# Kernel optimization log

Measured on AMD Instinct MI355X. Metric: run time of the kernel, lower is better.

The kernel has to match this reference:

```python
import jax, jax.numpy as jnp
import numpy as np

N, D_IN, D_OUT, RANK, MAX_LORAS = 4096, 2048, 2048, 16, 32


def setup_inputs() -> dict:
    key = jax.random.key(0)
    ks = jax.random.split(key, 6)
    x = jax.random.normal(ks[0], (N, D_IN), dtype=jnp.float32)
    adapter_ids = jax.random.randint(ks[1], (N,), 0, MAX_LORAS, dtype=jnp.int32)
    W_base = jax.random.normal(ks[2], (D_OUT, D_IN), dtype=jnp.float32) * (D_IN ** -0.5)
    b_base = jax.random.normal(ks[3], (D_OUT,), dtype=jnp.float32) * 0.01
    lora_A = jax.random.normal(ks[4], (MAX_LORAS, RANK, D_IN), dtype=jnp.float32) * (D_IN ** -0.5)
    lora_B = jax.random.normal(ks[5], (MAX_LORAS, D_OUT, RANK), dtype=jnp.float32) * (RANK ** -0.5)
    lora_scaling = jnp.ones((MAX_LORAS,), dtype=jnp.float32)
    return {"x": x, "adapter_ids": adapter_ids, "W_base": W_base, "b_base": b_base,
            "lora_A": lora_A, "lora_B": lora_B, "lora_scaling": lora_scaling}


def reference(x, adapter_ids, W_base, b_base, lora_A, lora_B, lora_scaling):
    previous_dtype = x.dtype
    # base_layer(x): dense Linear
    result = x @ W_base.T + b_base                      # [N, D_OUT]
    # lora_A(x, adapter_ids): per-token gathered low-rank down-projection (bgmv)
    A_w = lora_A[adapter_ids]                           # [N, RANK, D_IN]
    A_result = jnp.einsum('ni,nri->nr', x, A_w)         # [N, RANK]
    # lora_B(A_result, adapter_ids): per-token gathered up-projection
    B_w = lora_B[adapter_ids]                           # [N, D_OUT, RANK]
    B_result = jnp.einsum('nr,nor->no', A_result, B_w)  # [N, D_OUT]
    # scaled residual add, per-adapter scaling
    scaling = lora_scaling[adapter_ids][:, None]        # [N, 1]
    result = result + B_result * scaling
    # cast back to input dtype (skip_dtype_convert=False)
    return result.astype(previous_dtype)
```

## Files before the change

### kernel.cpp

```cpp
#include <hip/hip_runtime.h>
#include <hip/hip_bf16.h>
#include <stdint.h>

#define NTOK 4096
#define DIN  2048
#define DOUT 2048
#define RANK 16
#define NLORA 32
#define LCAP 512

typedef __attribute__((ext_vector_type(4))) float f32x4;
typedef __attribute__((ext_vector_type(8))) _Float16 f16x8;

typedef const __attribute__((address_space(1))) void* gas_ptr;
typedef __attribute__((address_space(3))) void* las_ptr;

__global__ __launch_bounds__(256)
void prep_kernel(const float* __restrict__ x, const int* __restrict__ ids,
                 const float* __restrict__ W, const float* __restrict__ lA,
                 const float* __restrict__ lB,
                 _Float16* __restrict__ xh, _Float16* __restrict__ wh,
                 _Float16* __restrict__ lAh, _Float16* __restrict__ lBh,
                 int* __restrict__ list, int* __restrict__ counts) {
    const int bid = blockIdx.x;
    if (bid < 7168) {
        const float* src; _Float16* dst; int lb;
        if      (bid < 2048) { src = W;  dst = wh;  lb = bid; }
        else if (bid < 6144) { src = x;  dst = xh;  lb = bid - 2048; }
        else if (bid < 6656) { src = lA; dst = lAh; lb = bid - 6144; }
        else                 { src = lB; dst = lBh; lb = bid - 6656; }
        const size_t i = ((size_t)lb * 256 + threadIdx.x) * 8;
        f32x4 a = *(const f32x4*)(src + i);
        f32x4 b = *(const f32x4*)(src + i + 4);
        f16x8 h;
        h[0] = (_Float16)a.x; h[1] = (_Float16)a.y; h[2] = (_Float16)a.z; h[3] = (_Float16)a.w;
        h[4] = (_Float16)b.x; h[5] = (_Float16)b.y; h[6] = (_Float16)b.z; h[7] = (_Float16)b.w;
        *(f16x8*)(dst + i) = h;
        return;
    }
    const int a = bid - 7168;
    const int wv = threadIdx.x >> 6;
    const int lane = threadIdx.x & 63;
    __shared__ int wcnt[4];
    int c = 0;
    for (int t0 = wv * 1024; t0 < wv * 1024 + 1024; t0 += 64)
        c += __popcll(__ballot(ids[t0 + lane] == a));
    if (lane == 0) wcnt[wv] = c;
    __syncthreads();
    int off = 0;
    for (int w = 0; w < wv; w++) off += wcnt[w];
    if (threadIdx.x == 0) counts[a] = wcnt[0] + wcnt[1] + wcnt[2] + wcnt[3];
    for (int t0 = wv * 1024; t0 < wv * 1024 + 1024; t0 += 64) {
        const int t = t0 + lane;
        const bool m = (ids[t] == a);
        unsigned long long bal = __ballot(m);
        if (m) {
            int pos = off + __popcll(bal & ((1ULL << lane) - 1));
            if (pos < LCAP) list[a * LCAP + pos] = t;
        }
        off += __popcll(bal);
    }
}

__global__ __launch_bounds__(512)
void lora_a_kernel(const _Float16* __restrict__ xh, const _Float16* __restrict__ lAh,
                   const float* __restrict__ scal, const int* __restrict__ list,
                   const int* __restrict__ counts, _Float16* __restrict__ aresh) {
    const int a = blockIdx.x, tile = blockIdx.y;
    const int cnt = counts[a];
    if (tile * 16 >= cnt) return;
    const int wave = threadIdx.x >> 6;
    const int lane = threadIdx.x & 63;
    const int fr = lane & 15, fq = lane >> 4;

    const int idxA = tile * 16 + fr;
    const int tA = (idxA < cnt) ? list[a * LCAP + idxA] : list[a * LCAP];

    const _Float16* xr = xh + (size_t)tA * DIN + wave * 256 + fq * 8;
    const _Float16* ar = lAh + (size_t)a * RANK * DIN + fr * DIN + wave * 256 + fq * 8;

    f32x4 acc = (f32x4){0.f, 0.f, 0.f, 0.f};
#pragma unroll
    for (int st = 0; st < 8; st++) {
        f16x8 af = *(const f16x8*)(xr + st * 32);
        f16x8 bf = *(const f16x8*)(ar + st * 32);
        acc = __builtin_amdgcn_mfma_f32_16x16x32_f16(af, bf, acc, 0, 0, 0);
    }

    __shared__ float red[8][256];
#pragma unroll
    for (int j = 0; j < 4; j++) red[wave][lane * 4 + j] = acc[j];
    __syncthreads();
    if (wave == 0) {
        const float s = scal[a];
#pragma unroll
        for (int j = 0; j < 4; j++) {
            float v = 0.f;
#pragma unroll
            for (int w = 0; w < 8; w++) v += red[w][lane * 4 + j];
            const int m = fq * 4 + j;
            const int idx = tile * 16 + m;
            if (idx < cnt) {
                const int t = list[a * LCAP + idx];
                aresh[(size_t)t * RANK + fr] = (_Float16)(v * s);
            }
        }
    }
}

__global__ __launch_bounds__(512)
void lora_b_kernel(const _Float16* __restrict__ aresh, const _Float16* __restrict__ lBh,
                   const float* __restrict__ bias, const int* __restrict__ list,
                   const int* __restrict__ counts, _Float16* __restrict__ Bresh) {
    const int a = blockIdx.x, tile = blockIdx.y;
    const int cnt = counts[a];
    if (tile * 16 >= cnt) return;
    const int wave = threadIdx.x >> 6;
    const int lane = threadIdx.x & 63;
    const int fr = lane & 15, fq = lane >> 4;

    const int idxA = tile * 16 + fr;
    const int tA = (idxA < cnt) ? list[a * LCAP + idxA] : list[a * LCAP];
    f16x8 af = {};
    if (fq < 2) af = *(const f16x8*)(aresh + (size_t)tA * RANK + fq * 8);

    int tj[4];
#pragma unroll
    for (int j = 0; j < 4; j++) {
        const int idx = tile * 16 + fq * 4 + j;
        tj[j] = (idx < cnt) ? list[a * LCAP + idx] : -1;
    }

    const _Float16* Bb = lBh + (size_t)a * DOUT * RANK;
    for (int oi = 0; oi < 16; oi++) {
        const int ot = oi * 8 + wave;
        const int o = ot * 16 + fr;
        f16x8 bf = {};
        if (fq < 2) bf = *(const f16x8*)(Bb + (size_t)o * RANK + fq * 8);
        f32x4 c = (f32x4){0.f, 0.f, 0.f, 0.f};
        c = __builtin_amdgcn_mfma_f32_16x16x32_f16(af, bf, c, 0, 0, 0);
        const float bv = bias[o];
#pragma unroll
        for (int j = 0; j < 4; j++)
            if (tj[j] >= 0) Bresh[(size_t)tj[j] * DOUT + o] = (_Float16)(c[j] + bv);
    }
}

#define BM 256
#define BN 128
#define BK 32

__global__ __launch_bounds__(512, 2)
void gemm_kernel(const _Float16* __restrict__ Ah, const _Float16* __restrict__ Wh,
                 const _Float16* __restrict__ Bresh, float* __restrict__ out) {
    extern __shared__ _Float16 sm[];
    _Float16* As = sm;
    _Float16* Bs = sm + 16384;

    const int tid = threadIdx.x;
    const int wave = tid >> 6;
    const int lane = tid & 63;
    const int wr = wave >> 1, wc = wave & 1;

    const int p = blockIdx.y * gridDim.x + blockIdx.x;
    const int L = (p & 7) * 32 + (p >> 3);
    const int bm = (L >> 4) * BM;
    const int bn = (L & 15) * BN;

    const int rsub = lane >> 2;
    const int cch = (lane & 3) ^ (rsub & 3);
    const _Float16* srcA[2];
    const _Float16* srcB;
    {
        const int rowA0 = (wave * 2 + 0) * 16 + rsub;
        const int rowA1 = (wave * 2 + 1) * 16 + rsub;
        srcA[0] = Ah + (size_t)(bm + rowA0) * DIN + cch * 8;
        srcA[1] = Ah + (size_t)(bm + rowA1) * DIN + cch * 8;
        const int rowB = wave * 16 + rsub;
        srcB = Wh + (size_t)(bn + rowB) * DIN + cch * 8;
    }

    const int fr = lane & 15;
    const int fq = lane >> 4;
    const int aoff = (wr * 64 + fr) * 32 + ((fq ^ (fr & 3)) * 8);
    const int boff = (wc * 64 + fr) * 32 + ((fq ^ (fr & 3)) * 8);

    f32x4 acc[4][4];
#pragma unroll
    for (int i = 0; i < 4; i++)
#pragma unroll
        for (int j = 0; j < 4; j++) acc[i][j] = (f32x4){0.f, 0.f, 0.f, 0.f};

#define STAGE(buf, koff)                                                                  \
    do {                                                                                  \
        __builtin_amdgcn_global_load_lds((gas_ptr)(srcA[0] + (koff)),                     \
            (las_ptr)(As + (buf) * 8192 + (wave * 2 + 0) * 512), 16, 0, 0);               \
        __builtin_amdgcn_global_load_lds((gas_ptr)(srcA[1] + (koff)),                     \
            (las_ptr)(As + (buf) * 8192 + (wave * 2 + 1) * 512), 16, 0, 0);               \
        __builtin_amdgcn_global_load_lds((gas_ptr)(srcB + (koff)),                        \
            (las_ptr)(Bs + (buf) * 4096 + wave * 512), 16, 0, 0);                         \
    } while (0)

    STAGE(0, 0);
    __syncthreads();

    for (int kt = 0; kt < DIN / BK; ++kt) {
        const int cur = kt & 1;
        if (kt < DIN / BK - 1) STAGE(cur ^ 1, (kt + 1) * BK);

        const _Float16* Ab = As + cur * 8192;
        const _Float16* Bb = Bs + cur * 4096;
        f16x8 ah[4], bh[4];
#pragma unroll
        for (int mi = 0; mi < 4; mi++) ah[mi] = *(const f16x8*)(Ab + aoff + mi * 512);
#pragma unroll
        for (int ni = 0; ni < 4; ni++) bh[ni] = *(const f16x8*)(Bb + boff + ni * 512);
#pragma unroll
        for (int mi = 0; mi < 4; mi++)
#pragma unroll
            for (int ni = 0; ni < 4; ni++)
                acc[mi][ni] = __builtin_amdgcn_mfma_f32_16x16x32_f16(ah[mi], bh[ni], acc[mi][ni], 0, 0, 0);
        __syncthreads();
    }

#pragma unroll
    for (int mi = 0; mi < 4; mi++) {
#pragma unroll
        for (int j = 0; j < 4; j++) {
            const int n = bm + wr * 64 + mi * 16 + fq * 4 + j;
#pragma unroll
            for (int ni = 0; ni < 4; ni++) {
                const int o = bn + wc * 64 + ni * 16 + fr;
                out[(size_t)n * DOUT + o] = acc[mi][ni][j] + (float)Bresh[(size_t)n * DOUT + o];
            }
        }
    }
}

extern "C" void kernel_launch(void* const* d_in, const int* in_sizes, int n_in,
                              void* d_out, int out_size, void* d_ws, size_t ws_size,
                              hipStream_t stream) {
    const float* x    = (const float*)d_in[0];
    const int*   ids  = (const int*)d_in[1];
    const float* W    = (const float*)d_in[2];
    const float* bias = (const float*)d_in[3];
    const float* lA   = (const float*)d_in[4];
    const float* lB   = (const float*)d_in[5];
    const float* scal = (const float*)d_in[6];
    float* out = (float*)d_out;

    _Float16* xh    = (_Float16*)d_ws;
    _Float16* wh    = xh + (size_t)NTOK * DIN;
    _Float16* lAh   = wh + (size_t)DOUT * DIN;
    _Float16* lBh   = lAh + (size_t)NLORA * RANK * DIN;
    _Float16* aresh = lBh + (size_t)NLORA * DOUT * RANK;
    _Float16* Bresh = aresh + (size_t)NTOK * RANK;
    int* list   = (int*)(Bresh + (size_t)NTOK * DOUT);
    int* counts = list + (size_t)NLORA * LCAP;

    prep_kernel<<<dim3(7168 + NLORA), 256, 0, stream>>>(
        x, ids, W, lA, lB, xh, wh, lAh, lBh, list, counts);
    lora_a_kernel<<<dim3(NLORA, 32), 512, 0, stream>>>(
        xh, lAh, scal, list, counts, aresh);
    lora_b_kernel<<<dim3(NLORA, 32), 512, 0, stream>>>(
        aresh, lBh, bias, list, counts, Bresh);
    gemm_kernel<<<dim3(16, 16), 512, 48 * 1024, stream>>>(
        xh, wh, Bresh, out);
}
```

Before: 177.7 us.

## Fuse LoRA A/B kernels and retile base GEMM to 128x128x64 with 256 threads

Merges the LoRA down- and up-projection kernels into one, keeping the rank-16 intermediate in shared memory instead of writing it to global memory. The change removes one launch and the global round trip for the intermediate. The base GEMM is retiled from 256x128 tiles with BK=32 and 512 threads to 128x128 tiles with BK=64 and 256 threads, using 512 blocks. It also switches to an XOR swizzle over 8 slots, explicit vmcnt waits with raw s_barrier, and setprio around the MFMA blocks. The partial vmcnt wait and barrier ordering add risk of races if the counts are wrong.

```diff
diff --git a/kernel.cpp b/kernel.cpp
--- a/kernel.cpp
+++ b/kernel.cpp
@@ -63,9 +63,10 @@
 }
 
 __global__ __launch_bounds__(512)
-void lora_a_kernel(const _Float16* __restrict__ xh, const _Float16* __restrict__ lAh,
-                   const float* __restrict__ scal, const int* __restrict__ list,
-                   const int* __restrict__ counts, _Float16* __restrict__ aresh) {
+void lora_fused_kernel(const _Float16* __restrict__ xh, const _Float16* __restrict__ lAh,
+                       const _Float16* __restrict__ lBh, const float* __restrict__ bias,
+                       const float* __restrict__ scal, const int* __restrict__ list,
+                       const int* __restrict__ counts, _Float16* __restrict__ Bresh) {
     const int a = blockIdx.x, tile = blockIdx.y;
     const int cnt = counts[a];
     if (tile * 16 >= cnt) return;
@@ -73,12 +74,14 @@
     const int lane = threadIdx.x & 63;
     const int fr = lane & 15, fq = lane >> 4;
 
+    __shared__ float red[8][256];
+    __shared__ _Float16 ares_h[16 * 16];
+
     const int idxA = tile * 16 + fr;
     const int tA = (idxA < cnt) ? list[a * LCAP + idxA] : list[a * LCAP];
 
     const _Float16* xr = xh + (size_t)tA * DIN + wave * 256 + fq * 8;
     const _Float16* ar = lAh + (size_t)a * RANK * DIN + fr * DIN + wave * 256 + fq * 8;
-
     f32x4 acc = (f32x4){0.f, 0.f, 0.f, 0.f};
 #pragma unroll
     for (int st = 0; st < 8; st++) {
@@ -86,8 +89,6 @@
         f16x8 bf = *(const f16x8*)(ar + st * 32);
         acc = __builtin_amdgcn_mfma_f32_16x16x32_f16(af, bf, acc, 0, 0, 0);
     }
-
-    __shared__ float red[8][256];
 #pragma unroll
     for (int j = 0; j < 4; j++) red[wave][lane * 4 + j] = acc[j];
     __syncthreads();
@@ -98,43 +99,23 @@
             float v = 0.f;
 #pragma unroll
             for (int w = 0; w < 8; w++) v += red[w][lane * 4 + j];
-            const int m = fq * 4 + j;
-            const int idx = tile * 16 + m;
-            if (idx < cnt) {
-                const int t = list[a * LCAP + idx];
-                aresh[(size_t)t * RANK + fr] = (_Float16)(v * s);
-            }
-        }
-    }
-}
-
-__global__ __launch_bounds__(512)
-void lora_b_kernel(const _Float16* __restrict__ aresh, const _Float16* __restrict__ lBh,
-                   const float* __restrict__ bias, const int* __restrict__ list,
-                   const int* __restrict__ counts, _Float16* __restrict__ Bresh) {
-    const int a = blockIdx.x, tile = blockIdx.y;
-    const int cnt = counts[a];
-    if (tile * 16 >= cnt) return;
-    const int wave = threadIdx.x >> 6;
-    const int lane = threadIdx.x & 63;
-    const int fr = lane & 15, fq = lane >> 4;
-
-    const int idxA = tile * 16 + fr;
-    const int tA = (idxA < cnt) ? list[a * LCAP + idxA] : list[a * LCAP];
+            ares_h[(fq * 4 + j) * RANK + fr] = (_Float16)(v * s);
+        }
+    }
+    __syncthreads();
+
     f16x8 af = {};
-    if (fq < 2) af = *(const f16x8*)(aresh + (size_t)tA * RANK + fq * 8);
-
+    if (fq < 2) af = *(const f16x8*)(ares_h + fr * RANK + fq * 8);
     int tj[4];
 #pragma unroll
     for (int j = 0; j < 4; j++) {
         const int idx = tile * 16 + fq * 4 + j;
         tj[j] = (idx < cnt) ? list[a * LCAP + idx] : -1;
     }
-
     const _Float16* Bb = lBh + (size_t)a * DOUT * RANK;
+#pragma unroll 4
     for (int oi = 0; oi < 16; oi++) {
-        const int ot = oi * 8 + wave;
-        const int o = ot * 16 + fr;
+        const int o = (wave * 16 + oi) * 16 + fr;
         f16x8 bf = {};
         if (fq < 2) bf = *(const f16x8*)(Bb + (size_t)o * RANK + fq * 8);
         f32x4 c = (f32x4){0.f, 0.f, 0.f, 0.f};
@@ -146,11 +127,10 @@
     }
 }
 
-#define BM 256
-#define BN 128
-#define BK 32
-
-__global__ __launch_bounds__(512, 2)
+#define GBK 64
+#define NT (DIN / GBK)
+
+__global__ __launch_bounds__(256, 2)
 void gemm_kernel(const _Float16* __restrict__ Ah, const _Float16* __restrict__ Wh,
                  const _Float16* __restrict__ Bresh, float* __restrict__ out) {
     extern __shared__ _Float16 sm[];
@@ -162,28 +142,24 @@
     const int lane = tid & 63;
     const int wr = wave >> 1, wc = wave & 1;
 
-    const int p = blockIdx.y * gridDim.x + blockIdx.x;
-    const int L = (p & 7) * 32 + (p >> 3);
-    const int bm = (L >> 4) * BM;
-    const int bn = (L & 15) * BN;
-
-    const int rsub = lane >> 2;
-    const int cch = (lane & 3) ^ (rsub & 3);
-    const _Float16* srcA[2];
-    const _Float16* srcB;
-    {
-        const int rowA0 = (wave * 2 + 0) * 16 + rsub;
-        const int rowA1 = (wave * 2 + 1) * 16 + rsub;
-        srcA[0] = Ah + (size_t)(bm + rowA0) * DIN + cch * 8;
-        srcA[1] = Ah + (size_t)(bm + rowA1) * DIN + cch * 8;
-        const int rowB = wave * 16 + rsub;
-        srcB = Wh + (size_t)(bn + rowB) * DIN + cch * 8;
+    const int p = blockIdx.x;
+    const int L = (p & 7) * 64 + (p >> 3);
+    const int bm = (L >> 4) * 128;
+    const int bn = (L & 15) * 128;
+
+    const int rsub = lane >> 3;
+    const int cch = (lane & 7) ^ rsub;
+    const _Float16* srcA[4];
+    const _Float16* srcB[4];
+#pragma unroll
+    for (int i = 0; i < 4; i++) {
+        const int row = (wave * 4 + i) * 8 + rsub;
+        srcA[i] = Ah + (size_t)(bm + row) * DIN + cch * 8;
+        srcB[i] = Wh + (size_t)(bn + row) * DIN + cch * 8;
     }
 
     const int fr = lane & 15;
     const int fq = lane >> 4;
-    const int aoff = (wr * 64 + fr) * 32 + ((fq ^ (fr & 3)) * 8);
-    const int boff = (wc * 64 + fr) * 32 + ((fq ^ (fr & 3)) * 8);
 
     f32x4 acc[4][4];
 #pragma unroll
@@ -193,34 +169,54 @@
 
 #define STAGE(buf, koff)                                                                  \
     do {                                                                                  \
-        __builtin_amdgcn_global_load_lds((gas_ptr)(srcA[0] + (koff)),                     \
-            (las_ptr)(As + (buf) * 8192 + (wave * 2 + 0) * 512), 16, 0, 0);               \
-        __builtin_amdgcn_global_load_lds((gas_ptr)(srcA[1] + (koff)),                     \
-            (las_ptr)(As + (buf) * 8192 + (wave * 2 + 1) * 512), 16, 0, 0);               \
-        __builtin_amdgcn_global_load_lds((gas_ptr)(srcB + (koff)),                        \
-            (las_ptr)(Bs + (buf) * 4096 + wave * 512), 16, 0, 0);                         \
+        _Pragma("unroll")                                                                 \
+        for (int i = 0; i < 4; i++) {                                                     \
+            __builtin_amdgcn_global_load_lds((gas_ptr)(srcA[i] + (koff)),                 \
+                (las_ptr)(As + (buf) * 8192 + (wave * 4 + i) * 512), 16, 0, 0);           \
+            __builtin_amdgcn_global_load_lds((gas_ptr)(srcB[i] + (koff)),                 \
+                (las_ptr)(Bs + (buf) * 8192 + (wave * 4 + i) * 512), 16, 0, 0);           \
+        }                                                                                 \
     } while (0)
 
     STAGE(0, 0);
-    __syncthreads();
-
-    for (int kt = 0; kt < DIN / BK; ++kt) {
+
+    for (int kt = 0; kt < NT; ++kt) {
         const int cur = kt & 1;
-        if (kt < DIN / BK - 1) STAGE(cur ^ 1, (kt + 1) * BK);
+        if (kt < NT - 1) {
+            STAGE(cur ^ 1, (kt + 1) * GBK);
+            asm volatile("s_waitcnt vmcnt(8)" ::: "memory");
+        } else {
+            asm volatile("s_waitcnt vmcnt(0)" ::: "memory");
+        }
+        __builtin_amdgcn_s_barrier();
+        __builtin_amdgcn_sched_barrier(0);
 
         const _Float16* Ab = As + cur * 8192;
-        const _Float16* Bb = Bs + cur * 4096;
-        f16x8 ah[4], bh[4];
-#pragma unroll
-        for (int mi = 0; mi < 4; mi++) ah[mi] = *(const f16x8*)(Ab + aoff + mi * 512);
-#pragma unroll
-        for (int ni = 0; ni < 4; ni++) bh[ni] = *(const f16x8*)(Bb + boff + ni * 512);
-#pragma unroll
-        for (int mi = 0; mi < 4; mi++)
-#pragma unroll
-            for (int ni = 0; ni < 4; ni++)
-                acc[mi][ni] = __builtin_amdgcn_mfma_f32_16x16x32_f16(ah[mi], bh[ni], acc[mi][ni], 0, 0, 0);
-        __syncthreads();
+        const _Float16* Bb = Bs + cur * 8192;
+#pragma unroll
+        for (int kk = 0; kk < 2; kk++) {
+            f16x8 av[4], bv[4];
+#pragma unroll
+            for (int mi = 0; mi < 4; mi++) {
+                const int row = wr * 64 + mi * 16 + fr;
+                const int slot = (kk * 4 + fq) ^ (row & 7);
+                av[mi] = *(const f16x8*)(Ab + row * 64 + slot * 8);
+            }
+#pragma unroll
+            for (int ni = 0; ni < 4; ni++) {
+                const int row = wc * 64 + ni * 16 + fr;
+                const int slot = (kk * 4 + fq) ^ (row & 7);
+                bv[ni] = *(const f16x8*)(Bb + row * 64 + slot * 8);
+            }
+            __builtin_amdgcn_s_setprio(1);
+#pragma unroll
+            for (int mi = 0; mi < 4; mi++)
+#pragma unroll
+                for (int ni = 0; ni < 4; ni++)
+                    acc[mi][ni] = __builtin_amdgcn_mfma_f32_16x16x32_f16(av[mi], bv[ni], acc[mi][ni], 0, 0, 0);
+            __builtin_amdgcn_s_setprio(0);
+        }
+        __builtin_amdgcn_s_barrier();
     }
 
 #pragma unroll
@@ -253,17 +249,14 @@
     _Float16* wh    = xh + (size_t)NTOK * DIN;
     _Float16* lAh   = wh + (size_t)DOUT * DIN;
     _Float16* lBh   = lAh + (size_t)NLORA * RANK * DIN;
-    _Float16* aresh = lBh + (size_t)NLORA * DOUT * RANK;
-    _Float16* Bresh = aresh + (size_t)NTOK * RANK;
+    _Float16* Bresh = lBh + (size_t)NLORA * DOUT * RANK;
     int* list   = (int*)(Bresh + (size_t)NTOK * DOUT);
     int* counts = list + (size_t)NLORA * LCAP;
 
     prep_kernel<<<dim3(7168 + NLORA), 256, 0, stream>>>(
         x, ids, W, lA, lB, xh, wh, lAh, lBh, list, counts);
-    lora_a_kernel<<<dim3(NLORA, 32), 512, 0, stream>>>(
-        xh, lAh, scal, list, counts, aresh);
-    lora_b_kernel<<<dim3(NLORA, 32), 512, 0, stream>>>(
-        aresh, lBh, bias, list, counts, Bresh);
-    gemm_kernel<<<dim3(16, 16), 512, 48 * 1024, stream>>>(
+    lora_fused_kernel<<<dim3(NLORA, 32), 512, 0, stream>>>(
+        xh, lAh, lBh, bias, scal, list, counts, Bresh);
+    gemm_kernel<<<dim3(512), 256, 64 * 1024, stream>>>(
         xh, wh, Bresh, out);
 }
```

Result: faster. 162.7 us (-8.4%).
